# Kernel tuning notes

Hardware: AMD Instinct MI355X
Metric: run time of the kernel (lower is better)

The kernel has to match this reference:

```python
import jax, jax.numpy as jnp
import numpy as np

B, D_IN, EXPERT_DIM, N_EXPERT, N_TASK = 16384, 1024, 256, 8, 4


def setup_inputs() -> dict:
    key = jax.random.key(0)
    k1, k2, k3 = jax.random.split(key, 3)
    x = jax.random.normal(k1, (B, D_IN), dtype=jnp.float32)
    # Glorot-ish scaling for weights
    We = jax.random.normal(k2, (N_EXPERT, D_IN, EXPERT_DIM), dtype=jnp.float32) * (1.0 / np.sqrt(D_IN))
    be = jnp.zeros((N_EXPERT, EXPERT_DIM), dtype=jnp.float32)
    Wg = jax.random.normal(k3, (N_TASK, D_IN, N_EXPERT), dtype=jnp.float32) * (1.0 / np.sqrt(D_IN))
    bg = jnp.zeros((N_TASK, N_EXPERT), dtype=jnp.float32)
    return {"x": x, "We": We, "be": be, "Wg": Wg, "bg": bg}


def reference(x, We, be, Wg, bg):
    # Experts: grouped GEMM -> [B, n_expert, expert_dim]
    E = jax.nn.relu(jnp.einsum("bd,edh->beh", x, We) + be[None, :, :])
    # Gates: [B, n_task, n_expert], softmax over experts
    G = jax.nn.softmax(jnp.einsum("bd,tde->bte", x, Wg) + bg[None, :, :], axis=-1)
    # Gated combine per task: towers[t] = E^T @ g_t -> [n_task, B, expert_dim]
    towers = jnp.einsum("beh,bte->tbh", E, G)
    return towers  # stacked version of the original list of [B, expert_dim] towers
```

## Files before the change

### kernel.cpp

```cpp
#include <hip/hip_runtime.h>

#define B_ROWS 16384
#define D_IN   1024
#define H_DIM  256
#define N_EXP  8
#define N_TASK 4
#define NKT    16

typedef short bf16x8 __attribute__((ext_vector_type(8)));
typedef float f32x4  __attribute__((ext_vector_type(4)));
typedef unsigned short u16x8 __attribute__((ext_vector_type(8)));

static __device__ __forceinline__ unsigned short f2bf(float f) {
  unsigned int u = __float_as_uint(f);
  u += 0x7fffu + ((u >> 16) & 1u);
  return (unsigned short)(u >> 16);
}

#define WS_XB   0u
#define WS_WET  33554432u
#define WS_WGT  37748736u
#define WS_GT   37814272u

__global__ void k_prep_w(const float* __restrict__ We, const float* __restrict__ Wg,
                         unsigned short* __restrict__ We_t, unsigned short* __restrict__ Wg_t) {
  int bid = blockIdx.x;
  int t = threadIdx.x;
  if (bid < 512) {
    int e = bid >> 6;
    int tl = bid & 63;
    int k0 = (tl >> 2) * 64, h0 = (tl & 3) * 64;
    __shared__ unsigned short tile[64][72];
    const float* src = We + (size_t)e * (D_IN * H_DIM);
#pragma unroll
    for (int i = 0; i < 4; ++i) {
      int kk = (t >> 4) + i * 16;
      int hh = (t & 15) * 4;
      float4 v = *(const float4*)(src + (size_t)(k0 + kk) * H_DIM + h0 + hh);
      tile[hh + 0][kk] = f2bf(v.x);
      tile[hh + 1][kk] = f2bf(v.y);
      tile[hh + 2][kk] = f2bf(v.z);
      tile[hh + 3][kk] = f2bf(v.w);
    }
    __syncthreads();
    unsigned short* dst = We_t + (size_t)e * (H_DIM * D_IN);
#pragma unroll
    for (int i = 0; i < 4; ++i) {
      int hh = (t >> 4) + i * 16;
      int kk = (t & 15) * 4;
      ushort4 u = *(const ushort4*)&tile[hh][kk];
      *(ushort4*)(dst + (size_t)(h0 + hh) * D_IN + k0 + kk) = u;
    }
  } else {
    int n = bid - 512;
    int tsk = n >> 3, e = n & 7;
    int k = t * 4;
    const float* src = Wg + (size_t)tsk * (D_IN * 8) + e;
    ushort4 u;
    u.x = f2bf(src[(size_t)(k + 0) * 8]);
    u.y = f2bf(src[(size_t)(k + 1) * 8]);
    u.z = f2bf(src[(size_t)(k + 2) * 8]);
    u.w = f2bf(src[(size_t)(k + 3) * 8]);
    *(ushort4*)(Wg_t + (size_t)n * D_IN + k) = u;
  }
}

__global__ __launch_bounds__(256) void k_gates(const float* __restrict__ x,
                                               const unsigned short* __restrict__ Wg_t,
                                               unsigned short* __restrict__ x_b,
                                               const float* __restrict__ bg,
                                               float* __restrict__ Gt) {
  __shared__ float red[4][16][36];
  int m0 = blockIdx.x * 16;
  int t = threadIdx.x;
  int w = t >> 6, l = t & 63;
  int lr = l & 15, lq = l >> 4;
  int kbase = w * 256;
  f32x4 acc0 = {0.f, 0.f, 0.f, 0.f}, acc1 = {0.f, 0.f, 0.f, 0.f};

  const float* xrow = x + (size_t)(m0 + lr) * D_IN;
  unsigned short* xbrow = x_b + (size_t)(m0 + lr) * D_IN;
  const unsigned short* wg0 = Wg_t + (size_t)lr * D_IN;
  const unsigned short* wg1 = Wg_t + (size_t)(16 + lr) * D_IN;

#pragma unroll
  for (int ks = 0; ks < 8; ++ks) {
    int k = kbase + ks * 32 + lq * 8;
    float4 v0 = *(const float4*)(xrow + k);
    float4 v1 = *(const float4*)(xrow + k + 4);
    bf16x8 a;
    a[0] = (short)f2bf(v0.x); a[1] = (short)f2bf(v0.y);
    a[2] = (short)f2bf(v0.z); a[3] = (short)f2bf(v0.w);
    a[4] = (short)f2bf(v1.x); a[5] = (short)f2bf(v1.y);
    a[6] = (short)f2bf(v1.z); a[7] = (short)f2bf(v1.w);
    *(bf16x8*)(xbrow + k) = a;
    bf16x8 b0 = *(const bf16x8*)(wg0 + k);
    bf16x8 b1 = *(const bf16x8*)(wg1 + k);
    acc0 = __builtin_amdgcn_mfma_f32_16x16x32_bf16(a, b0, acc0, 0, 0, 0);
    acc1 = __builtin_amdgcn_mfma_f32_16x16x32_bf16(a, b1, acc1, 0, 0, 0);
  }

#pragma unroll
  for (int j = 0; j < 4; ++j) {
    red[w][lq * 4 + j][lr]      = acc0[j];
    red[w][lq * 4 + j][16 + lr] = acc1[j];
  }
  __syncthreads();
  if (w == 0) {
#pragma unroll
    for (int j = 0; j < 4; ++j) {
      int rr = lq * 4 + j;
      acc0[j] = red[0][rr][lr] + red[1][rr][lr] + red[2][rr][lr] + red[3][rr][lr];
      acc1[j] = red[0][rr][16 + lr] + red[1][rr][16 + lr] + red[2][rr][16 + lr] + red[3][rr][16 + lr];
    }
    int colb = lr;
    int rbase = m0 + lq * 4;
    float bga = bg[colb], bgb = bg[16 + colb];
#pragma unroll
    for (int j = 0; j < 4; ++j) {
      float va = acc0[j] + bga;
      float vb = acc1[j] + bgb;
      float mxa = va, mxb = vb;
#pragma unroll
      for (int d = 1; d < 8; d <<= 1) {
        mxa = fmaxf(mxa, __shfl_xor(mxa, d));
        mxb = fmaxf(mxb, __shfl_xor(mxb, d));
      }
      va = __expf(va - mxa); vb = __expf(vb - mxb);
      float sa = va, sb = vb;
#pragma unroll
      for (int d = 1; d < 8; d <<= 1) {
        sa += __shfl_xor(sa, d);
        sb += __shfl_xor(sb, d);
      }
      va /= sa; vb /= sb;
      Gt[(size_t)colb * B_ROWS + rbase + j]        = va;
      Gt[(size_t)(16 + colb) * B_ROWS + rbase + j] = vb;
    }
  }
}

__global__ __launch_bounds__(512, 2) void k_expert(const unsigned short* __restrict__ x_b,
                                                   const unsigned short* __restrict__ We_t,
                                                   const float* __restrict__ be,
                                                   const float* __restrict__ Gt,
                                                   float* __restrict__ out) {
  __shared__ unsigned short As[2][256 * 64];
  __shared__ unsigned short Bs[2][256 * 64];
  int bid = blockIdx.x;
  int t = threadIdx.x;

  int xcd = bid & 7;
  int idx = bid >> 3;
  int m   = xcd * 8 + (idx >> 3);
  int hs  = idx & 7;
  int m0  = m * 256;

  int w  = t >> 6, l = t & 63;
  int wm = w >> 2, wn = w & 3;
  int lr = l & 15, lq = l >> 4;

  const unsigned short* Ab = x_b + (size_t)m0 * D_IN;

  const int sr = t >> 3, sg = t & 7;
  const int swz0 = ((lq ^ (lr & 7)) << 3);
  const int swz1 = (((4 + lq) ^ (lr & 7)) << 3);
  const int arow0 = (wm * 128 + lr) << 6;
  const int brow0 = (wn * 64 + lr) << 6;

  size_t bsrc[4];
#pragma unroll
  for (int q2 = 0; q2 < 4; ++q2) {
    int rq = q2 * 64 + sr;
    int me = (rq >> 3) & 7;
    int mh = hs * 32 + ((rq >> 6) & 3) * 8 + (rq & 7);
    bsrc[q2] = (size_t)(me * H_DIM + mh) * D_IN + (size_t)((sg ^ (rq & 7)) << 3);
  }

  f32x4 acc[8][4];
#pragma unroll
  for (int i = 0; i < 8; ++i)
#pragma unroll
    for (int j = 0; j < 4; ++j) acc[i][j] = (f32x4){0.f, 0.f, 0.f, 0.f};

#define STAGE_A(cb, kt, h)                                                                       \
  do {                                                                                           \
    int r0_ = (h) * 128 + sr;                                                                    \
    int r1_ = r0_ + 64;                                                                          \
    __builtin_amdgcn_global_load_lds(                                                            \
        (const __attribute__((address_space(1))) void*)(Ab + (size_t)r0_ * D_IN + (kt) * 64 +    \
                                                        ((sg ^ (r0_ & 7)) << 3)),                \
        (__attribute__((address_space(3))) void*)(&As[(cb)][r0_ * 64 + sg * 8]), 16, 0, 0);      \
    __builtin_amdgcn_global_load_lds(                                                            \
        (const __attribute__((address_space(1))) void*)(Ab + (size_t)r1_ * D_IN + (kt) * 64 +    \
                                                        ((sg ^ (r1_ & 7)) << 3)),                \
        (__attribute__((address_space(3))) void*)(&As[(cb)][r1_ * 64 + sg * 8]), 16, 0, 0);      \
  } while (0)
#define STAGE_B(cb, kt, h)                                                                       \
  do {                                                                                           \
    int r0_ = (h) * 128 + sr;                                                                    \
    int r1_ = r0_ + 64;                                                                          \
    __builtin_amdgcn_global_load_lds(                                                            \
        (const __attribute__((address_space(1))) void*)(We_t + bsrc[2 * (h)] + (kt) * 64),       \
        (__attribute__((address_space(3))) void*)(&Bs[(cb)][r0_ * 64 + sg * 8]), 16, 0, 0);      \
    __builtin_amdgcn_global_load_lds(                                                            \
        (const __attribute__((address_space(1))) void*)(We_t + bsrc[2 * (h) + 1] + (kt) * 64),   \
        (__attribute__((address_space(3))) void*)(&Bs[(cb)][r1_ * 64 + sg * 8]), 16, 0, 0);      \
  } while (0)

  STAGE_A(0, 0, 0); STAGE_A(0, 0, 1);
  STAGE_B(0, 0, 0); STAGE_B(0, 0, 1);
  STAGE_B(1, 1, 0); STAGE_B(1, 1, 1);
  asm volatile("s_waitcnt vmcnt(4)" ::: "memory");
  __builtin_amdgcn_s_barrier();

#pragma unroll 2
  for (int kt = 0; kt < NKT; ++kt) {
    int c = kt & 1;
    const unsigned short* Ap = &As[c][0];
    const unsigned short* Bp = &Bs[c][0];
    bf16x8 b0[4], b1[4];
#pragma unroll
    for (int q = 0; q < 4; ++q) {
      if (q == 0) {
#pragma unroll
        for (int fn = 0; fn < 4; ++fn) {
          b0[fn] = *(const bf16x8*)(Bp + brow0 + fn * 1024 + swz0);
          b1[fn] = *(const bf16x8*)(Bp + brow0 + fn * 1024 + swz1);
        }
      }
      bf16x8 a00 = *(const bf16x8*)(Ap + arow0 + (2 * q) * 1024 + swz0);
      bf16x8 a01 = *(const bf16x8*)(Ap + arow0 + (2 * q) * 1024 + swz1);
      bf16x8 a10 = *(const bf16x8*)(Ap + arow0 + (2 * q + 1) * 1024 + swz0);
      bf16x8 a11 = *(const bf16x8*)(Ap + arow0 + (2 * q + 1) * 1024 + swz1);
      if (q == 0)      { if (kt + 1 < NKT) STAGE_A(c ^ 1, kt + 1, 0); }
      else if (q == 1) { if (kt + 1 < NKT) STAGE_A(c ^ 1, kt + 1, 1); }
      else if (q == 2) { if (kt + 2 < NKT) STAGE_B(c, kt + 2, 0); }
      else             { if (kt + 2 < NKT) STAGE_B(c, kt + 2, 1); }
      __builtin_amdgcn_s_barrier();
      asm volatile("s_waitcnt lgkmcnt(0)" ::: "memory");
      __builtin_amdgcn_s_setprio(1);
#pragma unroll
      for (int fn = 0; fn < 4; ++fn) {
        acc[2 * q][fn]     = __builtin_amdgcn_mfma_f32_16x16x32_bf16(a00, b0[fn], acc[2 * q][fn], 0, 0, 0);
        acc[2 * q][fn]     = __builtin_amdgcn_mfma_f32_16x16x32_bf16(a01, b1[fn], acc[2 * q][fn], 0, 0, 0);
        acc[2 * q + 1][fn] = __builtin_amdgcn_mfma_f32_16x16x32_bf16(a10, b0[fn], acc[2 * q + 1][fn], 0, 0, 0);
        acc[2 * q + 1][fn] = __builtin_amdgcn_mfma_f32_16x16x32_bf16(a11, b1[fn], acc[2 * q + 1][fn], 0, 0, 0);
      }
      __builtin_amdgcn_s_setprio(0);
      if (q == 3) {
        if (kt < NKT - 2)        asm volatile("s_waitcnt vmcnt(4)" ::: "memory");
        else if (kt == NKT - 2)  asm volatile("s_waitcnt vmcnt(0)" ::: "memory");
      }
      __builtin_amdgcn_s_barrier();
    }
  }
#undef STAGE_A
#undef STAGE_B

  int hi = lr >> 3, h7 = lr & 7;
  int hglob = hs * 32 + wn * 8 + h7;
  float bev[4];
#pragma unroll
  for (int fn = 0; fn < 4; ++fn)
    bev[fn] = be[(2 * fn + hi) * H_DIM + hglob];
#pragma unroll
  for (int fm = 0; fm < 8; ++fm) {
    int r0 = m0 + wm * 128 + fm * 16 + lq * 4;
    float vv[4][4];
#pragma unroll
    for (int fn = 0; fn < 4; ++fn)
#pragma unroll
      for (int j = 0; j < 4; ++j)
        vv[fn][j] = fmaxf(acc[fm][fn][j] + bev[fn], 0.f);
    float p[4][4];
#pragma unroll
    for (int tk = 0; tk < 4; ++tk) {
      f32x4 gv[4];
#pragma unroll
      for (int fn = 0; fn < 4; ++fn)
        gv[fn] = *(const f32x4*)(Gt + (size_t)(tk * 8 + 2 * fn + hi) * B_ROWS + r0);
#pragma unroll
      for (int j = 0; j < 4; ++j)
        p[tk][j] = gv[0][j] * vv[0][j] + gv[1][j] * vv[1][j] +
                   gv[2][j] * vv[2][j] + gv[3][j] * vv[3][j];
    }
#pragma unroll
    for (int j = 0; j < 4; ++j) {
      float sa = hi ? p[0][j] : p[2][j];
      float sb = hi ? p[1][j] : p[3][j];
      float ra = __shfl_xor(sa, 8);
      float rb = __shfl_xor(sb, 8);
      float t0 = (hi ? p[2][j] : p[0][j]) + ra;
      float t1 = (hi ? p[3][j] : p[1][j]) + rb;
      size_t tk0 = (size_t)(hi * 2);
      out[(tk0 * B_ROWS + r0 + j) * H_DIM + hglob]       = t0;
      out[((tk0 + 1) * B_ROWS + r0 + j) * H_DIM + hglob] = t1;
    }
  }
}

extern "C" void kernel_launch(void* const* d_in, const int* in_sizes, int n_in,
                              void* d_out, int out_size, void* d_ws, size_t ws_size,
                              hipStream_t stream) {
  const float* x  = (const float*)d_in[0];
  const float* We = (const float*)d_in[1];
  const float* be = (const float*)d_in[2];
  const float* Wg = (const float*)d_in[3];
  const float* bg = (const float*)d_in[4];
  float* out = (float*)d_out;
  char* ws = (char*)d_ws;
  unsigned short* x_b  = (unsigned short*)(ws + WS_XB);
  unsigned short* We_t = (unsigned short*)(ws + WS_WET);
  unsigned short* Wg_t = (unsigned short*)(ws + WS_WGT);
  float*          Gt   = (float*)(ws + WS_GT);

  k_prep_w<<<544, 256, 0, stream>>>(We, Wg, We_t, Wg_t);
  k_gates<<<B_ROWS / 16, 256, 0, stream>>>(x, Wg_t, x_b, bg, Gt);
  k_expert<<<512, 512, 0, stream>>>(x_b, We_t, be, Gt, out);
}
```

Before: 209.3 us.

## Fuse gate computation into expert kernel and merge x conversion into prep

Removes the separate gates kernel. The fp32-to-bf16 conversion of x moves into the weight-prep launch as extra blocks. Each expert block now computes the gate logits and softmax for its own 256 rows with MFMA before the main GEMM, then stages them in shared memory for the epilogue instead of reading a global Gt buffer. This saves a kernel launch and the Gt global round trip, but the gate GEMM is recomputed by all 8 h-slice blocks that share the same rows, and its accumulators add register pressure to the expert kernel.

```diff
diff --git a/kernel.cpp b/kernel.cpp
--- a/kernel.cpp
+++ b/kernel.cpp
@@ -20,9 +20,10 @@
 #define WS_XB   0u
 #define WS_WET  33554432u
 #define WS_WGT  37748736u
-#define WS_GT   37814272u
-
-__global__ void k_prep_w(const float* __restrict__ We, const float* __restrict__ Wg,
+
+__global__ void k_prep_w(const float* __restrict__ x, const float* __restrict__ We,
+                         const float* __restrict__ Wg,
+                         unsigned short* __restrict__ x_b,
                          unsigned short* __restrict__ We_t, unsigned short* __restrict__ Wg_t) {
   int bid = blockIdx.x;
   int t = threadIdx.x;
@@ -51,7 +52,7 @@
       ushort4 u = *(const ushort4*)&tile[hh][kk];
       *(ushort4*)(dst + (size_t)(h0 + hh) * D_IN + k0 + kk) = u;
     }
-  } else {
+  } else if (bid < 544) {
     int n = bid - 512;
     int tsk = n >> 3, e = n & 7;
     int k = t * 4;
@@ -62,88 +63,24 @@
     u.z = f2bf(src[(size_t)(k + 2) * 8]);
     u.w = f2bf(src[(size_t)(k + 3) * 8]);
     *(ushort4*)(Wg_t + (size_t)n * D_IN + k) = u;
-  }
-}
-
-__global__ __launch_bounds__(256) void k_gates(const float* __restrict__ x,
-                                               const unsigned short* __restrict__ Wg_t,
-                                               unsigned short* __restrict__ x_b,
-                                               const float* __restrict__ bg,
-                                               float* __restrict__ Gt) {
-  __shared__ float red[4][16][36];
-  int m0 = blockIdx.x * 16;
-  int t = threadIdx.x;
-  int w = t >> 6, l = t & 63;
-  int lr = l & 15, lq = l >> 4;
-  int kbase = w * 256;
-  f32x4 acc0 = {0.f, 0.f, 0.f, 0.f}, acc1 = {0.f, 0.f, 0.f, 0.f};
-
-  const float* xrow = x + (size_t)(m0 + lr) * D_IN;
-  unsigned short* xbrow = x_b + (size_t)(m0 + lr) * D_IN;
-  const unsigned short* wg0 = Wg_t + (size_t)lr * D_IN;
-  const unsigned short* wg1 = Wg_t + (size_t)(16 + lr) * D_IN;
-
-#pragma unroll
-  for (int ks = 0; ks < 8; ++ks) {
-    int k = kbase + ks * 32 + lq * 8;
-    float4 v0 = *(const float4*)(xrow + k);
-    float4 v1 = *(const float4*)(xrow + k + 4);
-    bf16x8 a;
-    a[0] = (short)f2bf(v0.x); a[1] = (short)f2bf(v0.y);
-    a[2] = (short)f2bf(v0.z); a[3] = (short)f2bf(v0.w);
-    a[4] = (short)f2bf(v1.x); a[5] = (short)f2bf(v1.y);
-    a[6] = (short)f2bf(v1.z); a[7] = (short)f2bf(v1.w);
-    *(bf16x8*)(xbrow + k) = a;
-    bf16x8 b0 = *(const bf16x8*)(wg0 + k);
-    bf16x8 b1 = *(const bf16x8*)(wg1 + k);
-    acc0 = __builtin_amdgcn_mfma_f32_16x16x32_bf16(a, b0, acc0, 0, 0, 0);
-    acc1 = __builtin_amdgcn_mfma_f32_16x16x32_bf16(a, b1, acc1, 0, 0, 0);
-  }
-
-#pragma unroll
-  for (int j = 0; j < 4; ++j) {
-    red[w][lq * 4 + j][lr]      = acc0[j];
-    red[w][lq * 4 + j][16 + lr] = acc1[j];
-  }
-  __syncthreads();
-  if (w == 0) {
-#pragma unroll
-    for (int j = 0; j < 4; ++j) {
-      int rr = lq * 4 + j;
-      acc0[j] = red[0][rr][lr] + red[1][rr][lr] + red[2][rr][lr] + red[3][rr][lr];
-      acc1[j] = red[0][rr][16 + lr] + red[1][rr][16 + lr] + red[2][rr][16 + lr] + red[3][rr][16 + lr];
-    }
-    int colb = lr;
-    int rbase = m0 + lq * 4;
-    float bga = bg[colb], bgb = bg[16 + colb];
-#pragma unroll
-    for (int j = 0; j < 4; ++j) {
-      float va = acc0[j] + bga;
-      float vb = acc1[j] + bgb;
-      float mxa = va, mxb = vb;
-#pragma unroll
-      for (int d = 1; d < 8; d <<= 1) {
-        mxa = fmaxf(mxa, __shfl_xor(mxa, d));
-        mxb = fmaxf(mxb, __shfl_xor(mxb, d));
-      }
-      va = __expf(va - mxa); vb = __expf(vb - mxb);
-      float sa = va, sb = vb;
-#pragma unroll
-      for (int d = 1; d < 8; d <<= 1) {
-        sa += __shfl_xor(sa, d);
-        sb += __shfl_xor(sb, d);
-      }
-      va /= sa; vb /= sb;
-      Gt[(size_t)colb * B_ROWS + rbase + j]        = va;
-      Gt[(size_t)(16 + colb) * B_ROWS + rbase + j] = vb;
-    }
+  } else {
+    size_t base = (size_t)(bid - 544) * 2048 + (size_t)t * 8;
+    float4 v0 = *(const float4*)(x + base);
+    float4 v1 = *(const float4*)(x + base + 4);
+    u16x8 u;
+    u[0] = f2bf(v0.x); u[1] = f2bf(v0.y);
+    u[2] = f2bf(v0.z); u[3] = f2bf(v0.w);
+    u[4] = f2bf(v1.x); u[5] = f2bf(v1.y);
+    u[6] = f2bf(v1.z); u[7] = f2bf(v1.w);
+    *(u16x8*)(x_b + base) = u;
   }
 }
 
 __global__ __launch_bounds__(512, 2) void k_expert(const unsigned short* __restrict__ x_b,
                                                    const unsigned short* __restrict__ We_t,
+                                                   const unsigned short* __restrict__ Wg_t,
                                                    const float* __restrict__ be,
-                                                   const float* __restrict__ Gt,
+                                                   const float* __restrict__ bg,
                                                    float* __restrict__ out) {
   __shared__ unsigned short As[2][256 * 64];
   __shared__ unsigned short Bs[2][256 * 64];
@@ -161,6 +98,54 @@
   int lr = l & 15, lq = l >> 4;
 
   const unsigned short* Ab = x_b + (size_t)m0 * D_IN;
+
+  f32x4 ga[2][2];
+#pragma unroll
+  for (int rg = 0; rg < 2; ++rg)
+#pragma unroll
+    for (int cg = 0; cg < 2; ++cg) ga[rg][cg] = (f32x4){0.f, 0.f, 0.f, 0.f};
+  {
+    const unsigned short* xg0 = Ab + (size_t)(w * 32 + lr) * D_IN;
+    const unsigned short* xg1 = Ab + (size_t)(w * 32 + 16 + lr) * D_IN;
+    const unsigned short* wg0 = Wg_t + (size_t)lr * D_IN;
+    const unsigned short* wg1 = Wg_t + (size_t)(16 + lr) * D_IN;
+#pragma unroll 4
+    for (int ko = 0; ko < 32; ++ko) {
+      int k = ko * 32 + lq * 8;
+      bf16x8 a0 = *(const bf16x8*)(xg0 + k);
+      bf16x8 a1 = *(const bf16x8*)(xg1 + k);
+      bf16x8 b0 = *(const bf16x8*)(wg0 + k);
+      bf16x8 b1 = *(const bf16x8*)(wg1 + k);
+      ga[0][0] = __builtin_amdgcn_mfma_f32_16x16x32_bf16(a0, b0, ga[0][0], 0, 0, 0);
+      ga[0][1] = __builtin_amdgcn_mfma_f32_16x16x32_bf16(a0, b1, ga[0][1], 0, 0, 0);
+      ga[1][0] = __builtin_amdgcn_mfma_f32_16x16x32_bf16(a1, b0, ga[1][0], 0, 0, 0);
+      ga[1][1] = __builtin_amdgcn_mfma_f32_16x16x32_bf16(a1, b1, ga[1][1], 0, 0, 0);
+    }
+    float bga = bg[lr], bgb = bg[16 + lr];
+#pragma unroll
+    for (int rg = 0; rg < 2; ++rg) {
+#pragma unroll
+      for (int j = 0; j < 4; ++j) {
+        float va = ga[rg][0][j] + bga;
+        float vb = ga[rg][1][j] + bgb;
+        float mxa = va, mxb = vb;
+#pragma unroll
+        for (int d = 1; d < 8; d <<= 1) {
+          mxa = fmaxf(mxa, __shfl_xor(mxa, d));
+          mxb = fmaxf(mxb, __shfl_xor(mxb, d));
+        }
+        va = __expf(va - mxa); vb = __expf(vb - mxb);
+        float sa = va, sb = vb;
+#pragma unroll
+        for (int d = 1; d < 8; d <<= 1) {
+          sa += __shfl_xor(sa, d);
+          sb += __shfl_xor(sb, d);
+        }
+        ga[rg][0][j] = va / sa;
+        ga[rg][1][j] = vb / sb;
+      }
+    }
+  }
 
   const int sr = t >> 3, sg = t & 7;
   const int swz0 = ((lq ^ (lr & 7)) << 3);
@@ -258,6 +243,17 @@
 #undef STAGE_A
 #undef STAGE_B
 
+  float (*Gl)[260] = (float (*)[260])(&As[0][0]);
+#pragma unroll
+  for (int rg = 0; rg < 2; ++rg)
+#pragma unroll
+    for (int j = 0; j < 4; ++j) {
+      int rloc = w * 32 + rg * 16 + lq * 4 + j;
+      Gl[lr][rloc]      = ga[rg][0][j];
+      Gl[16 + lr][rloc] = ga[rg][1][j];
+    }
+  __syncthreads();
+
   int hi = lr >> 3, h7 = lr & 7;
   int hglob = hs * 32 + wn * 8 + h7;
   float bev[4];
@@ -266,7 +262,8 @@
     bev[fn] = be[(2 * fn + hi) * H_DIM + hglob];
 #pragma unroll
   for (int fm = 0; fm < 8; ++fm) {
-    int r0 = m0 + wm * 128 + fm * 16 + lq * 4;
+    int rloc = wm * 128 + fm * 16 + lq * 4;
+    int r0 = m0 + rloc;
     float vv[4][4];
 #pragma unroll
     for (int fn = 0; fn < 4; ++fn)
@@ -279,7 +276,7 @@
       f32x4 gv[4];
 #pragma unroll
       for (int fn = 0; fn < 4; ++fn)
-        gv[fn] = *(const f32x4*)(Gt + (size_t)(tk * 8 + 2 * fn + hi) * B_ROWS + r0);
+        gv[fn] = *(const f32x4*)&Gl[tk * 8 + 2 * fn + hi][rloc];
 #pragma unroll
       for (int j = 0; j < 4; ++j)
         p[tk][j] = gv[0][j] * vv[0][j] + gv[1][j] * vv[1][j] +
@@ -313,9 +310,7 @@
   unsigned short* x_b  = (unsigned short*)(ws + WS_XB);
   unsigned short* We_t = (unsigned short*)(ws + WS_WET);
   unsigned short* Wg_t = (unsigned short*)(ws + WS_WGT);
-  float*          Gt   = (float*)(ws + WS_GT);
-
-  k_prep_w<<<544, 256, 0, stream>>>(We, Wg, We_t, Wg_t);
-  k_gates<<<B_ROWS / 16, 256, 0, stream>>>(x, Wg_t, x_b, bg, Gt);
-  k_expert<<<512, 512, 0, stream>>>(x_b, We_t, be, Gt, out);
+
+  k_prep_w<<<544 + 8192, 256, 0, stream>>>(x, We, Wg, x_b, We_t, Wg_t);
+  k_expert<<<512, 512, 0, stream>>>(x_b, We_t, Wg_t, be, bg, out);
 }
```

Result: slower. 252.5 us (+20.6%).
